# Optimization experiments

Measured on AMD Instinct MI355X. Metric: run time of the kernel, lower is better.

The kernel has to match this reference:

```python
import jax, jax.numpy as jnp
import numpy as np
import math

N_HEAD = 16
N_HEAD_KV = 4
HEAD_DIM = 128
N_EMBD = 2048

def alibi_slopes(n_heads):
    def pow2_slopes(n):
        start = 2 ** (-2 ** (-(math.log2(n) - 3)))
        return [start * start ** i for i in range(n)]
    if math.log2(n_heads).is_integer():
        return jnp.array(pow2_slopes(n_heads), dtype=jnp.float32)
    closest = 2 ** math.floor(math.log2(n_heads))
    base = pow2_slopes(closest)
    if n_heads <= 2 * closest:
        s = base + base[0::2]
    else:
        s = base + base[0::2] + base[1::2]
    return jnp.array(s[:n_heads], dtype=jnp.float32)

def setup_inputs() -> dict:
    key = jax.random.key(0)
    ks = jax.random.split(key, 5)
    B, T, C = 2, 2048, N_EMBD
    kvdim = N_HEAD_KV * HEAD_DIM
    sc = 0.02
    return {
        "x": jax.random.normal(ks[0], (B, T, C), dtype=jnp.float32),
        "q_w": jax.random.normal(ks[1], (C, C), dtype=jnp.float32) * sc,
        "k_w": jax.random.normal(ks[2], (kvdim, C), dtype=jnp.float32) * sc,
        "v_w": jax.random.normal(ks[3], (kvdim, C), dtype=jnp.float32) * sc,
        "o_w": jax.random.normal(ks[4], (C, C), dtype=jnp.float32) * sc,
    }

def reference(x, q_w, k_w, v_w, o_w):
    B, T, C = x.shape
    H, Hkv, D = N_HEAD, N_HEAD_KV, HEAD_DIM
    # nan/inf sanitize (no-op for random inputs, kept for fidelity)
    x = jnp.nan_to_num(x, nan=0.0, posinf=10000.0, neginf=-10000.0)
    q = (x @ q_w.T).reshape(B, T, H, D).transpose(0, 2, 1, 3)      # [B,H,T,D]
    k = (x @ k_w.T).reshape(B, T, Hkv, D).transpose(0, 2, 1, 3)    # [B,Hkv,T,D]
    v = (x @ v_w.T).reshape(B, T, Hkv, D).transpose(0, 2, 1, 3)
    # repeat_interleave KV heads to H heads
    rep = H // Hkv
    k = jnp.repeat(k, rep, axis=1)
    v = jnp.repeat(v, rep, axis=1)
    scale = 1.0 / math.sqrt(D)
    att = jnp.einsum('bhqd,bhkd->bhqk', q, k) * scale
    att = jnp.clip(att, -10000.0, 10000.0)
    pos = jnp.arange(T)
    causal = jnp.where(pos[None, :] > pos[:, None], -jnp.inf, 0.0)  # [T,T]
    slopes = alibi_slopes(H)  # [H]
    rel = (pos[None, :] - pos[:, None]).astype(jnp.float32)         # [T,T]
    alibi = slopes[:, None, None] * rel[None]                        # [H,T,T]
    att = att + causal[None, None] + alibi[None]
    att = jax.nn.softmax(att.astype(jnp.float32), axis=-1).astype(q.dtype)
    y = jnp.einsum('bhqk,bhkd->bhqd', att, v)
    y = jnp.nan_to_num(y, nan=0.0, posinf=10000.0, neginf=-10000.0)
    y = y.transpose(0, 2, 1, 3).reshape(B, T, C)
    return y @ o_w.T
```

## Files before the change

kernel.cpp:

```cpp
#include <hip/hip_runtime.h>
#include <hip/hip_bf16.h>
#include <math.h>

#define SEQ   2048
#define EMBD  2048
#define NH    16
#define NKV   4
#define HD    128
#define NQKV  3072
#define NUNITS 512

typedef __attribute__((ext_vector_type(8))) short short8;
typedef __attribute__((ext_vector_type(4))) short short4v;
typedef __attribute__((ext_vector_type(4))) float floatx4;

static __device__ __forceinline__ short f2bf(float f) {
    union { float f; unsigned u; } cv; cv.f = f;
    unsigned u = cv.u;
    u += 0x7FFF + ((u >> 16) & 1);
    return (short)(u >> 16);
}

#define GL16(gsrc, ldst)                                                        \
    __builtin_amdgcn_global_load_lds(                                           \
        (const __attribute__((address_space(1))) void*)(gsrc),                  \
        (__attribute__((address_space(3))) void*)(ldst), 16, 0, 0)

static __device__ __forceinline__ int alibi_window(float slope2) {
    return (int)ceilf((42.0f / slope2 + 63.0f) * (1.0f / 64.0f));
}

static __device__ __forceinline__ int unit_cost(int h, int p) {
    float slope2 = exp2f(-0.5f * (float)(h + 1)) * 1.44269504f;
    int W = alibi_window(slope2);
    return min(W + 1, 2 * p + 2);
}

__global__ void cvt_all(const float* __restrict__ x,  const float* __restrict__ qw,
                        const float* __restrict__ kw, const float* __restrict__ vw,
                        const float* __restrict__ ow,
                        short* __restrict__ xb, short* __restrict__ wall,
                        short* __restrict__ owb) {
    int i = blockIdx.x * blockDim.x + threadIdx.x;
    const float* src; short* dst; int off;
    if (i < 2097152)      { src = x;  dst = xb;             off = i; }
    else if (i < 3145728) { src = qw; dst = wall;           off = i - 2097152; }
    else if (i < 3407872) { src = kw; dst = wall + 4194304; off = i - 3145728; }
    else if (i < 3670016) { src = vw; dst = wall + 5242880; off = i - 3407872; }
    else                  { src = ow; dst = owb;            off = i - 3670016; }
    float4 v = ((const float4*)src)[off];
    float a[4] = {v.x, v.y, v.z, v.w};
    short4v o;
#pragma unroll
    for (int j = 0; j < 4; ++j) {
        float f = a[j];
        f = isnan(f) ? 0.0f : fminf(fmaxf(f, -10000.0f), 10000.0f);
        o[j] = f2bf(f);
    }
    ((short4v*)dst)[off] = o;
}

__global__ void attn_setup(int* __restrict__ qtab) {
    __shared__ int keys[NUNITS];
    int i = threadIdx.x;
    int hp = i >> 1;
    int key = unit_cost(hp >> 4, hp & 15) * 1024 + i;
    keys[i] = key;
    __syncthreads();
    int rank = 0;
    for (int j = 0; j < NUNITS; ++j) rank += (keys[j] > key);
    qtab[rank] = i;
}

template<int MODE>
__global__ __launch_bounds__(256) void gemm_bt(
    const short* __restrict__ A, const short* __restrict__ W,
    float* __restrict__ Cout, int M, int N, int K,
    short* __restrict__ qb, short* __restrict__ kb, short* __restrict__ vb)
{
    __shared__ __align__(16) short sA[128 * 64];
    __shared__ __align__(16) short sB[128 * 64];

    const int tid  = threadIdx.x;
    const int lane = tid & 63;
    const int wv   = tid >> 6;
    const int wr   = wv >> 1, wc = wv & 1;
    const int lr   = lane & 15, lg = lane >> 4;
    const int bn   = blockIdx.x, bm = blockIdx.y;

    const short* gA[4]; const short* gB[4];
    short* lA[4]; short* lB[4];
#pragma unroll
    for (int s = 0; s < 4; ++s) {
        int ck  = wv * 256 + s * 64 + lane;
        int row = ck >> 3, seg = ck & 7;
        int segSw = seg ^ (row & 7);
        gA[s] = A + (size_t)(bm * 128 + row) * K + segSw * 8;
        gB[s] = W + (size_t)(bn * 128 + row) * K + segSw * 8;
        lA[s] = &sA[(wv * 256 + s * 64) * 8];
        lB[s] = &sB[(wv * 256 + s * 64) * 8];
    }

    floatx4 acc[4][4] = {};
    const int nkt = K / 64;
    for (int kt = 0; kt < nkt; ++kt) {
#pragma unroll
        for (int s = 0; s < 4; ++s) {
            GL16(gA[s] + kt * 64, lA[s]);
            GL16(gB[s] + kt * 64, lB[s]);
        }
        __syncthreads();

#pragma unroll
        for (int ks = 0; ks < 2; ++ks) {
            short8 af[4], bfr[4];
#pragma unroll
            for (int i = 0; i < 4; ++i) {
                int ra = wr * 64 + i * 16 + lr;
                int rb = wc * 64 + i * 16 + lr;
                af[i]  = *(const short8*)&sA[ra * 64 + (((ks * 4 + lg) ^ (ra & 7)) * 8)];
                bfr[i] = *(const short8*)&sB[rb * 64 + (((ks * 4 + lg) ^ (rb & 7)) * 8)];
            }
#pragma unroll
            for (int i = 0; i < 4; ++i)
#pragma unroll
                for (int j = 0; j < 4; ++j)
                    acc[i][j] = __builtin_amdgcn_mfma_f32_16x16x32_bf16(af[i], bfr[j], acc[i][j], 0, 0, 0);
        }
        __syncthreads();
    }

    const float QSCALE = 0.08838834764831845f * 1.44269504f;
#pragma unroll
    for (int i = 0; i < 4; ++i)
#pragma unroll
        for (int j = 0; j < 4; ++j)
#pragma unroll
            for (int r = 0; r < 4; ++r) {
                int gm = bm * 128 + wr * 64 + i * 16 + lg * 4 + r;
                int gn = bn * 128 + wc * 64 + j * 16 + lr;
                float v = acc[i][j][r];
                if (MODE == 0) {
                    int b = gm >> 11, t = gm & (SEQ - 1);
                    if (gn < 2048) {
                        int h = gn >> 7, d = gn & 127;
                        qb[(((size_t)(b * NH + h)) * SEQ + t) * HD + d] = f2bf(v * QSCALE);
                    } else if (gn < 2560) {
                        int hk = (gn - 2048) >> 7, d = gn & 127;
                        kb[(((size_t)(b * NKV + hk)) * SEQ + t) * HD + d] = f2bf(v);
                    } else {
                        int hv = (gn - 2560) >> 7, d = gn & 127;
                        vb[(((size_t)(b * NKV + hv)) * HD + d) * SEQ + t] = f2bf(v);
                    }
                } else {
                    Cout[(size_t)gm * N + gn] = v;
                }
            }
}

__global__ __launch_bounds__(512, 4) void attn_fwd(
    const short* __restrict__ Q, const short* __restrict__ Kg,
    const short* __restrict__ VT, short* __restrict__ Y,
    const int* __restrict__ qtab)
{
    __shared__ __align__(16) short sK[2][64 * 128];
    __shared__ __align__(16) short sV[128 * 64];
    __shared__ short Plds[8][16][72];

    const int tid  = threadIdx.x;
    const int wave = tid >> 6, lane = tid & 63;
    const int lr = lane & 15, lg = lane >> 4;
    const int bid = blockIdx.x;

    const int rank = (bid < 256) ? bid : (767 - bid);
    const int uu = qtab[rank];
    const int b = uu & 1, hp = uu >> 1;
    const int h = hp >> 4, p = hp & 15;
    const int hkv = h >> 2;
    const int qgw = 2 * p + (wave < 4 ? 1 : 0);

    const short* Qb = Q  +  ((size_t)(b * NH  + h  )) * SEQ * HD;
    const short* Kp = Kg +  ((size_t)(b * NKV + hkv)) * SEQ * HD;
    const short* Vp = VT +  ((size_t)(b * NKV + hkv)) * HD * SEQ;

    const float slope2 = exp2f(-0.5f * (float)(h + 1)) * 1.44269504f;
    const int W = alibi_window(slope2);
    const int thi = 2 * p + 1;
    int tlo = thi - W; if (tlo < 0) tlo = 0;

    const short* gK[2]; const short* gV[2];
    int lOff[2];
#pragma unroll
    for (int j = 0; j < 2; ++j) {
        int ck = wave * 128 + j * 64 + lane;
        int krow = ck >> 4, kseg = ck & 15;
        gK[j] = Kp + (size_t)krow * HD + (kseg ^ (krow & 7)) * 8;
        int vrow = ck >> 3, vseg = ck & 7;
        gV[j] = Vp + (size_t)vrow * SEQ + (vseg ^ (vrow & 7)) * 8;
        lOff[j] = (wave * 128 + j * 64) * 8;
    }

    float c_nt[4];
#pragma unroll
    for (int nt = 0; nt < 4; ++nt) c_nt[nt] = slope2 * (float)(nt * 16 + lr);

    const int q0 = qgw * 64 + (wave & 3) * 16;
    short8 qf[4];
#pragma unroll
    for (int cc = 0; cc < 4; ++cc)
        qf[cc] = *(const short8*)&Qb[(size_t)(q0 + lr) * HD + cc * 32 + lg * 8];

    floatx4 po[8] = {};
    float m[4], lsum[4];
#pragma unroll
    for (int r = 0; r < 4; ++r) { m[r] = -3.0e38f; lsum[r] = 0.0f; }

    int cur = 0;
#pragma unroll
    for (int j = 0; j < 2; ++j)
        GL16(gK[j] + (size_t)(thi << 6) * HD, &sK[0][0] + lOff[j]);
    __syncthreads();

#pragma unroll 1
    for (int t = thi; t >= tlo; --t) {
#pragma unroll
        for (int j = 0; j < 2; ++j)
            GL16(gV[j] + (t << 6), &sV[0] + lOff[j]);
        if (t > tlo) {
#pragma unroll
            for (int j = 0; j < 2; ++j)
                GL16(gK[j] + (size_t)((t - 1) << 6) * HD, &sK[cur ^ 1][0] + lOff[j]);
        }

        const bool active = (t <= qgw) && (t > qgw - W);
        const int kv0 = t << 6;

        if (active) {
            const short* kr = &sK[cur][0];
            floatx4 sf[4];
            __builtin_amdgcn_s_setprio(1);
#pragma unroll
            for (int nt = 0; nt < 4; ++nt) {
                floatx4 sacc = {0.f, 0.f, 0.f, 0.f};
#pragma unroll
                for (int cc = 0; cc < 4; ++cc) {
                    int krow = nt * 16 + lr;
                    short8 kf = *(const short8*)&kr[krow * 128 + (((cc * 4 + lg) ^ (krow & 7)) * 8)];
                    sacc = __builtin_amdgcn_mfma_f32_16x16x32_bf16(qf[cc], kf, sacc, 0, 0, 0);
                }
                sf[nt] = sacc;
            }
            __builtin_amdgcn_s_setprio(0);

            const float a2t = slope2 * (float)kv0;
            const bool masked = (t == qgw);
#pragma unroll
            for (int r = 0; r < 4; ++r) {
                const int qpos = q0 + lg * 4 + r;
                float sv[4];
#pragma unroll
                for (int nt = 0; nt < 4; ++nt)
                    sv[nt] = sf[nt][r] + a2t + c_nt[nt];
                if (masked) {
#pragma unroll
                    for (int nt = 0; nt < 4; ++nt) {
                        int kpos = kv0 + nt * 16 + lr;
                        if (kpos > qpos) sv[nt] = -3.0e38f;
                    }
                }
                bool over = (sv[0] > m[r]) | (sv[1] > m[r]) | (sv[2] > m[r]) | (sv[3] > m[r]);
                if (__any(over)) {
                    float mx = fmaxf(fmaxf(sv[0], sv[1]), fmaxf(sv[2], sv[3]));
#pragma unroll
                    for (int off = 1; off < 16; off <<= 1) mx = fmaxf(mx, __shfl_xor(mx, off));
                    float mn = fmaxf(m[r], mx);
                    float rs = exp2f(m[r] - mn);
                    lsum[r] *= rs;
#pragma unroll
                    for (int dt = 0; dt < 8; ++dt) po[dt][r] *= rs;
                    m[r] = mn;
                }
#pragma unroll
                for (int nt = 0; nt < 4; ++nt) {
                    float pp = exp2f(sv[nt] - m[r]);
                    lsum[r] += pp;
                    Plds[wave][lg * 4 + r][nt * 16 + lr] = f2bf(pp);
                }
            }
        }

        __syncthreads();

        if (active) {
            short8 pf0 = *(const short8*)&Plds[wave][lr][lg * 8];
            short8 pf1 = *(const short8*)&Plds[wave][lr][32 + lg * 8];
            __builtin_amdgcn_s_setprio(1);
#pragma unroll
            for (int dt = 0; dt < 8; ++dt) {
                int vrow = dt * 16 + lr;
                short8 vf0 = *(const short8*)&sV[vrow * 64 + (((lg    ) ^ (vrow & 7)) * 8)];
                short8 vf1 = *(const short8*)&sV[vrow * 64 + (((lg + 4) ^ (vrow & 7)) * 8)];
                po[dt] = __builtin_amdgcn_mfma_f32_16x16x32_bf16(pf0, vf0, po[dt], 0, 0, 0);
                po[dt] = __builtin_amdgcn_mfma_f32_16x16x32_bf16(pf1, vf1, po[dt], 0, 0, 0);
            }
            __builtin_amdgcn_s_setprio(0);
        }

        __syncthreads();
        cur ^= 1;
    }

#pragma unroll
    for (int r = 0; r < 4; ++r) {
        float sum = lsum[r];
#pragma unroll
        for (int off = 1; off < 16; off <<= 1) sum += __shfl_xor(sum, off);
        float inv = 1.0f / sum;
        int row = q0 + lg * 4 + r;
#pragma unroll
        for (int dt = 0; dt < 8; ++dt)
            Y[((size_t)(b * SEQ + row)) * EMBD + h * HD + dt * 16 + lr] = f2bf(po[dt][r] * inv);
    }
}

extern "C" void kernel_launch(void* const* d_in, const int* in_sizes, int n_in,
                              void* d_out, int out_size, void* d_ws, size_t ws_size,
                              hipStream_t stream) {
    const float* x   = (const float*)d_in[0];
    const float* q_w = (const float*)d_in[1];
    const float* k_w = (const float*)d_in[2];
    const float* v_w = (const float*)d_in[3];
    const float* o_w = (const float*)d_in[4];
    float* out = (float*)d_out;

    char* ws = (char*)d_ws;
    short* x_bf  = (short*)(ws);
    short* w_all = (short*)(ws + 16777216);
    short* o_wb  = (short*)(ws + 29360128);
    short* q_b   = (short*)(ws + 37748736);
    short* k_b   = (short*)(ws + 54525952);
    short* vT_b  = (short*)(ws + 58720256);
    short* y_b   = (short*)(ws + 62914560);
    int*   qtab  = (int*)(ws);

    cvt_all<<<18432, 256, 0, stream>>>(x, q_w, k_w, v_w, o_w, x_bf, w_all, o_wb);

    gemm_bt<0><<<dim3(NQKV / 128, 4096 / 128), 256, 0, stream>>>(
        x_bf, w_all, nullptr, 4096, NQKV, EMBD, q_b, k_b, vT_b);

    attn_setup<<<1, NUNITS, 0, stream>>>(qtab);
    attn_fwd<<<512, 512, 0, stream>>>(q_b, k_b, vT_b, y_b, qtab);

    gemm_bt<1><<<dim3(EMBD / 128, 4096 / 128), 256, 0, stream>>>(
        y_b, o_wb, out, 4096, EMBD, EMBD, nullptr, nullptr, nullptr);
}
```

Measured before the change: 213.2 us.

## Split long attention units across KV and schedule them via a persistent atomic queue

The heaviest attention work units (heads with the widest ALiBi windows at late query positions) are split into two KV halves. Each half writes unnormalized partial output plus running max and sum to a workspace buffer, and a new combine kernel merges the halves. The attention kernel becomes persistent: blocks pull cost-sorted units from an atomic counter instead of using a fixed block-to-unit mapping. The goal is to shorten the load-imbalance tail, at the cost of an extra launch, partial-result traffic and atomic dispatch overhead.

```diff
diff --git a/kernel.cpp b/kernel.cpp
--- a/kernel.cpp
+++ b/kernel.cpp
@@ -8,7 +8,7 @@
 #define NKV   4
 #define HD    128
 #define NQKV  3072
-#define NUNITS 512
+#define NUNITS 584
 
 typedef __attribute__((ext_vector_type(8))) short short8;
 typedef __attribute__((ext_vector_type(4))) short short4v;
@@ -28,12 +28,6 @@
 
 static __device__ __forceinline__ int alibi_window(float slope2) {
     return (int)ceilf((42.0f / slope2 + 63.0f) * (1.0f / 64.0f));
-}
-
-static __device__ __forceinline__ int unit_cost(int h, int p) {
-    float slope2 = exp2f(-0.5f * (float)(h + 1)) * 1.44269504f;
-    int W = alibi_window(slope2);
-    return min(W + 1, 2 * p + 2);
 }
 
 __global__ void cvt_all(const float* __restrict__ x,  const float* __restrict__ qw,
@@ -62,14 +56,29 @@
 
 __global__ void attn_setup(int* __restrict__ qtab) {
     __shared__ int keys[NUNITS];
-    int i = threadIdx.x;
-    int hp = i >> 1;
-    int key = unit_cost(hp >> 4, hp & 15) * 1024 + i;
-    keys[i] = key;
+    const int i = threadIdx.x;
+    int key = 0, enc = 0;
+    if (i < NUNITS) {
+        int b, h, p, c;
+        if (i < 512) { b = i >> 8; h = (i >> 4) & 15; p = i & 15; c = 0; }
+        else { int j = i - 512; b = j / 36; int r2 = j % 36; h = 10 + r2 / 6; p = 10 + r2 % 6; c = 1; }
+        float slope2 = exp2f(-0.5f * (float)(h + 1)) * 1.44269504f;
+        int W = alibi_window(slope2);
+        int L = min(W + 1, 2 * p + 2);
+        bool split = (h >= 10) && (p >= 10);
+        int n0 = (L + 1) >> 1;
+        int cost = split ? (c == 0 ? n0 : L - n0) : L;
+        enc = (c << 9) | (b << 8) | (h << 4) | p;
+        key = cost * 1024 + i;
+        keys[i] = key;
+    }
     __syncthreads();
-    int rank = 0;
-    for (int j = 0; j < NUNITS; ++j) rank += (keys[j] > key);
-    qtab[rank] = i;
+    if (i < NUNITS) {
+        int rank = 0;
+        for (int j = 0; j < NUNITS; ++j) rank += (keys[j] > key);
+        qtab[rank] = enc;
+    }
+    if (i == 0) qtab[NUNITS] = 0;
 }
 
 template<int MODE>
@@ -161,166 +170,222 @@
 __global__ __launch_bounds__(512, 4) void attn_fwd(
     const short* __restrict__ Q, const short* __restrict__ Kg,
     const short* __restrict__ VT, short* __restrict__ Y,
-    const int* __restrict__ qtab)
+    float* __restrict__ part, int* __restrict__ qtab)
 {
     __shared__ __align__(16) short sK[2][64 * 128];
     __shared__ __align__(16) short sV[128 * 64];
     __shared__ short Plds[8][16][72];
+    __shared__ int s_unit;
 
     const int tid  = threadIdx.x;
     const int wave = tid >> 6, lane = tid & 63;
     const int lr = lane & 15, lg = lane >> 4;
-    const int bid = blockIdx.x;
-
-    const int rank = (bid < 256) ? bid : (767 - bid);
-    const int uu = qtab[rank];
-    const int b = uu & 1, hp = uu >> 1;
-    const int h = hp >> 4, p = hp & 15;
-    const int hkv = h >> 2;
-    const int qgw = 2 * p + (wave < 4 ? 1 : 0);
-
-    const short* Qb = Q  +  ((size_t)(b * NH  + h  )) * SEQ * HD;
-    const short* Kp = Kg +  ((size_t)(b * NKV + hkv)) * SEQ * HD;
-    const short* Vp = VT +  ((size_t)(b * NKV + hkv)) * HD * SEQ;
-
-    const float slope2 = exp2f(-0.5f * (float)(h + 1)) * 1.44269504f;
-    const int W = alibi_window(slope2);
-    const int thi = 2 * p + 1;
-    int tlo = thi - W; if (tlo < 0) tlo = 0;
-
-    const short* gK[2]; const short* gV[2];
+    int* qcnt = qtab + NUNITS;
+
     int lOff[2];
 #pragma unroll
-    for (int j = 0; j < 2; ++j) {
-        int ck = wave * 128 + j * 64 + lane;
-        int krow = ck >> 4, kseg = ck & 15;
-        gK[j] = Kp + (size_t)krow * HD + (kseg ^ (krow & 7)) * 8;
-        int vrow = ck >> 3, vseg = ck & 7;
-        gV[j] = Vp + (size_t)vrow * SEQ + (vseg ^ (vrow & 7)) * 8;
-        lOff[j] = (wave * 128 + j * 64) * 8;
-    }
-
-    float c_nt[4];
-#pragma unroll
-    for (int nt = 0; nt < 4; ++nt) c_nt[nt] = slope2 * (float)(nt * 16 + lr);
-
-    const int q0 = qgw * 64 + (wave & 3) * 16;
-    short8 qf[4];
-#pragma unroll
-    for (int cc = 0; cc < 4; ++cc)
-        qf[cc] = *(const short8*)&Qb[(size_t)(q0 + lr) * HD + cc * 32 + lg * 8];
-
-    floatx4 po[8] = {};
-    float m[4], lsum[4];
-#pragma unroll
-    for (int r = 0; r < 4; ++r) { m[r] = -3.0e38f; lsum[r] = 0.0f; }
-
-    int cur = 0;
-#pragma unroll
     for (int j = 0; j < 2; ++j)
-        GL16(gK[j] + (size_t)(thi << 6) * HD, &sK[0][0] + lOff[j]);
-    __syncthreads();
+        lOff[j] = (wave * 128 + j * 64 + lane) * 8;
+
+    for (;;) {
+        if (tid == 0) {
+            int r = atomicAdd(qcnt, 1);
+            s_unit = (r < NUNITS) ? qtab[r] : -1;
+        }
+        __syncthreads();
+        const int enc = s_unit;
+        __syncthreads();
+        if (enc < 0) break;
+
+        const int c = (enc >> 9) & 1, b = (enc >> 8) & 1;
+        const int h = (enc >> 4) & 15, p = enc & 15;
+        const int hkv = h >> 2;
+        const int qgw = 2 * p + (wave < 4 ? 1 : 0);
+
+        const short* Qb = Q  +  ((size_t)(b * NH  + h  )) * SEQ * HD;
+        const short* Kp = Kg +  ((size_t)(b * NKV + hkv)) * SEQ * HD;
+        const short* Vp = VT +  ((size_t)(b * NKV + hkv)) * HD * SEQ;
+
+        const float slope2 = exp2f(-0.5f * (float)(h + 1)) * 1.44269504f;
+        const int W = alibi_window(slope2);
+        const int thi = 2 * p + 1;
+        const int L = min(W + 1, 2 * p + 2);
+        const bool split = (h >= 10) && (p >= 10);
+        const int n0 = (L + 1) >> 1;
+        int t1, t0;
+        if (!split)      { t1 = thi;      t0 = thi - L + 1; }
+        else if (c == 0) { t1 = thi;      t0 = thi - n0 + 1; }
+        else             { t1 = thi - n0; t0 = thi - L + 1; }
+
+        const short* gK[2]; const short* gV[2];
+#pragma unroll
+        for (int j = 0; j < 2; ++j) {
+            int ck = wave * 128 + j * 64 + lane;
+            int krow = ck >> 4, kseg = ck & 15;
+            gK[j] = Kp + (size_t)krow * HD + (kseg ^ (krow & 7)) * 8;
+            int vrow = ck >> 3, vseg = ck & 7;
+            gV[j] = Vp + (size_t)vrow * SEQ + (vseg ^ (vrow & 7)) * 8;
+        }
+
+        float c_nt[4];
+#pragma unroll
+        for (int nt = 0; nt < 4; ++nt) c_nt[nt] = slope2 * (float)(nt * 16 + lr);
+
+        const int q0 = qgw * 64 + (wave & 3) * 16;
+        short8 qf[4];
+#pragma unroll
+        for (int cc = 0; cc < 4; ++cc)
+            qf[cc] = *(const short8*)&Qb[(size_t)(q0 + lr) * HD + cc * 32 + lg * 8];
+
+        floatx4 po[8] = {};
+        float m[4], lsum[4];
+#pragma unroll
+        for (int r = 0; r < 4; ++r) { m[r] = -3.0e38f; lsum[r] = 0.0f; }
+
+        int cur = 0;
+#pragma unroll
+        for (int j = 0; j < 2; ++j)
+            GL16(gK[j] + (size_t)(t1 << 6) * HD, &sK[0][0] + lOff[j]);
+        __syncthreads();
 
 #pragma unroll 1
-    for (int t = thi; t >= tlo; --t) {
-#pragma unroll
-        for (int j = 0; j < 2; ++j)
-            GL16(gV[j] + (t << 6), &sV[0] + lOff[j]);
-        if (t > tlo) {
+        for (int t = t1; t >= t0; --t) {
 #pragma unroll
             for (int j = 0; j < 2; ++j)
-                GL16(gK[j] + (size_t)((t - 1) << 6) * HD, &sK[cur ^ 1][0] + lOff[j]);
-        }
-
-        const bool active = (t <= qgw) && (t > qgw - W);
-        const int kv0 = t << 6;
-
-        if (active) {
-            const short* kr = &sK[cur][0];
-            floatx4 sf[4];
-            __builtin_amdgcn_s_setprio(1);
-#pragma unroll
-            for (int nt = 0; nt < 4; ++nt) {
-                floatx4 sacc = {0.f, 0.f, 0.f, 0.f};
-#pragma unroll
-                for (int cc = 0; cc < 4; ++cc) {
-                    int krow = nt * 16 + lr;
-                    short8 kf = *(const short8*)&kr[krow * 128 + (((cc * 4 + lg) ^ (krow & 7)) * 8)];
-                    sacc = __builtin_amdgcn_mfma_f32_16x16x32_bf16(qf[cc], kf, sacc, 0, 0, 0);
+                GL16(gV[j] + (t << 6), &sV[0] + lOff[j]);
+            if (t > t0) {
+#pragma unroll
+                for (int j = 0; j < 2; ++j)
+                    GL16(gK[j] + (size_t)((t - 1) << 6) * HD, &sK[cur ^ 1][0] + lOff[j]);
+            }
+
+            const bool active = (t <= qgw) && (t > qgw - W);
+            const int kv0 = t << 6;
+
+            if (active) {
+                const short* kr = &sK[cur][0];
+                floatx4 sf[4];
+                __builtin_amdgcn_s_setprio(1);
+#pragma unroll
+                for (int nt = 0; nt < 4; ++nt) {
+                    floatx4 sacc = {0.f, 0.f, 0.f, 0.f};
+#pragma unroll
+                    for (int cc = 0; cc < 4; ++cc) {
+                        int krow = nt * 16 + lr;
+                        short8 kf = *(const short8*)&kr[krow * 128 + (((cc * 4 + lg) ^ (krow & 7)) * 8)];
+                        sacc = __builtin_amdgcn_mfma_f32_16x16x32_bf16(qf[cc], kf, sacc, 0, 0, 0);
+                    }
+                    sf[nt] = sacc;
                 }
-                sf[nt] = sacc;
-            }
-            __builtin_amdgcn_s_setprio(0);
-
-            const float a2t = slope2 * (float)kv0;
-            const bool masked = (t == qgw);
-#pragma unroll
-            for (int r = 0; r < 4; ++r) {
-                const int qpos = q0 + lg * 4 + r;
-                float sv[4];
-#pragma unroll
-                for (int nt = 0; nt < 4; ++nt)
-                    sv[nt] = sf[nt][r] + a2t + c_nt[nt];
-                if (masked) {
+                __builtin_amdgcn_s_setprio(0);
+
+                const float a2t = slope2 * (float)kv0;
+                const bool masked = (t == qgw);
+#pragma unroll
+                for (int r = 0; r < 4; ++r) {
+                    const int qpos = q0 + lg * 4 + r;
+                    float sv[4];
+#pragma unroll
+                    for (int nt = 0; nt < 4; ++nt)
+                        sv[nt] = sf[nt][r] + a2t + c_nt[nt];
+                    if (masked) {
+#pragma unroll
+                        for (int nt = 0; nt < 4; ++nt) {
+                            int kpos = kv0 + nt * 16 + lr;
+                            if (kpos > qpos) sv[nt] = -3.0e38f;
+                        }
+                    }
+                    bool over = (sv[0] > m[r]) | (sv[1] > m[r]) | (sv[2] > m[r]) | (sv[3] > m[r]);
+                    if (__any(over)) {
+                        float mx = fmaxf(fmaxf(sv[0], sv[1]), fmaxf(sv[2], sv[3]));
+#pragma unroll
+                        for (int off = 1; off < 16; off <<= 1) mx = fmaxf(mx, __shfl_xor(mx, off));
+                        float mn = fmaxf(m[r], mx);
+                        float rs = exp2f(m[r] - mn);
+                        lsum[r] *= rs;
+#pragma unroll
+                        for (int dt = 0; dt < 8; ++dt) po[dt][r] *= rs;
+                        m[r] = mn;
+                    }
 #pragma unroll
                     for (int nt = 0; nt < 4; ++nt) {
-                        int kpos = kv0 + nt * 16 + lr;
-                        if (kpos > qpos) sv[nt] = -3.0e38f;
+                        float pp = exp2f(sv[nt] - m[r]);
+                        lsum[r] += pp;
+                        Plds[wave][lg * 4 + r][nt * 16 + lr] = f2bf(pp);
                     }
                 }
-                bool over = (sv[0] > m[r]) | (sv[1] > m[r]) | (sv[2] > m[r]) | (sv[3] > m[r]);
-                if (__any(over)) {
-                    float mx = fmaxf(fmaxf(sv[0], sv[1]), fmaxf(sv[2], sv[3]));
-#pragma unroll
-                    for (int off = 1; off < 16; off <<= 1) mx = fmaxf(mx, __shfl_xor(mx, off));
-                    float mn = fmaxf(m[r], mx);
-                    float rs = exp2f(m[r] - mn);
-                    lsum[r] *= rs;
-#pragma unroll
-                    for (int dt = 0; dt < 8; ++dt) po[dt][r] *= rs;
-                    m[r] = mn;
+            }
+
+            __syncthreads();
+
+            if (active) {
+                short8 pf0 = *(const short8*)&Plds[wave][lr][lg * 8];
+                short8 pf1 = *(const short8*)&Plds[wave][lr][32 + lg * 8];
+                __builtin_amdgcn_s_setprio(1);
+#pragma unroll
+                for (int dt = 0; dt < 8; ++dt) {
+                    int vrow = dt * 16 + lr;
+                    short8 vf0 = *(const short8*)&sV[vrow * 64 + (((lg    ) ^ (vrow & 7)) * 8)];
+                    short8 vf1 = *(const short8*)&sV[vrow * 64 + (((lg + 4) ^ (vrow & 7)) * 8)];
+                    po[dt] = __builtin_amdgcn_mfma_f32_16x16x32_bf16(pf0, vf0, po[dt], 0, 0, 0);
+                    po[dt] = __builtin_amdgcn_mfma_f32_16x16x32_bf16(pf1, vf1, po[dt], 0, 0, 0);
                 }
-#pragma unroll
-                for (int nt = 0; nt < 4; ++nt) {
-                    float pp = exp2f(sv[nt] - m[r]);
-                    lsum[r] += pp;
-                    Plds[wave][lg * 4 + r][nt * 16 + lr] = f2bf(pp);
-                }
-            }
-        }
-
-        __syncthreads();
-
-        if (active) {
-            short8 pf0 = *(const short8*)&Plds[wave][lr][lg * 8];
-            short8 pf1 = *(const short8*)&Plds[wave][lr][32 + lg * 8];
-            __builtin_amdgcn_s_setprio(1);
-#pragma unroll
-            for (int dt = 0; dt < 8; ++dt) {
-                int vrow = dt * 16 + lr;
-                short8 vf0 = *(const short8*)&sV[vrow * 64 + (((lg    ) ^ (vrow & 7)) * 8)];
-                short8 vf1 = *(const short8*)&sV[vrow * 64 + (((lg + 4) ^ (vrow & 7)) * 8)];
-                po[dt] = __builtin_amdgcn_mfma_f32_16x16x32_bf16(pf0, vf0, po[dt], 0, 0, 0);
-                po[dt] = __builtin_amdgcn_mfma_f32_16x16x32_bf16(pf1, vf1, po[dt], 0, 0, 0);
-            }
-            __builtin_amdgcn_s_setprio(0);
-        }
-
-        __syncthreads();
-        cur ^= 1;
-    }
-
-#pragma unroll
-    for (int r = 0; r < 4; ++r) {
-        float sum = lsum[r];
-#pragma unroll
-        for (int off = 1; off < 16; off <<= 1) sum += __shfl_xor(sum, off);
-        float inv = 1.0f / sum;
-        int row = q0 + lg * 4 + r;
-#pragma unroll
-        for (int dt = 0; dt < 8; ++dt)
-            Y[((size_t)(b * SEQ + row)) * EMBD + h * HD + dt * 16 + lr] = f2bf(po[dt][r] * inv);
-    }
+                __builtin_amdgcn_s_setprio(0);
+            }
+
+            __syncthreads();
+            cur ^= 1;
+        }
+
+        if (!split) {
+#pragma unroll
+            for (int r = 0; r < 4; ++r) {
+                float sum = lsum[r];
+#pragma unroll
+                for (int off = 1; off < 16; off <<= 1) sum += __shfl_xor(sum, off);
+                float inv = 1.0f / sum;
+                int row = q0 + lg * 4 + r;
+#pragma unroll
+                for (int dt = 0; dt < 8; ++dt)
+                    Y[((size_t)(b * SEQ + row)) * EMBD + h * HD + dt * 16 + lr] = f2bf(po[dt][r] * inv);
+            }
+        } else {
+            int jslot = b * 36 + (h - 10) * 6 + (p - 10);
+            float* pw = part + (size_t)(jslot * 2 + c) * (128 * 130);
+#pragma unroll
+            for (int r = 0; r < 4; ++r) {
+                float sum = lsum[r];
+#pragma unroll
+                for (int off = 1; off < 16; off <<= 1) sum += __shfl_xor(sum, off);
+                int rr = wave * 16 + lg * 4 + r;
+#pragma unroll
+                for (int dt = 0; dt < 8; ++dt)
+                    pw[rr * 130 + dt * 16 + lr] = po[dt][r];
+                if (lr == 0) { pw[rr * 130 + 128] = m[r]; pw[rr * 130 + 129] = sum; }
+            }
+        }
+    }
+}
+
+__global__ void attn_combine(const float* __restrict__ part, short* __restrict__ Y) {
+    const int tid = threadIdx.x;
+    const int rg  = blockIdx.x * 2 + (tid >> 7);
+    const int col = tid & 127;
+    const int j = rg >> 7, rr = rg & 127;
+    const int b = j / 36; const int r2 = j % 36;
+    const int h = 10 + r2 / 6, p = 10 + r2 % 6;
+
+    const float* p0 = part + ((size_t)(j * 2) * 128 + rr) * 130;
+    const float* p1 = p0 + 128 * 130;
+    float m0 = p0[128], l0 = p0[129];
+    float m1 = p1[128], l1 = p1[129];
+    float M = fmaxf(m0, m1);
+    float s0 = exp2f(m0 - M), s1 = exp2f(m1 - M);
+    float v = (p0[col] * s0 + p1[col] * s1) / (l0 * s0 + l1 * s1);
+
+    const int w = rr >> 4, i2 = rr & 15;
+    const int grow = (w < 4 ? (2 * p + 1) : (2 * p)) * 64 + (w & 3) * 16 + i2;
+    Y[((size_t)(b * SEQ + grow)) * EMBD + h * HD + col] = f2bf(v);
 }
 
 extern "C" void kernel_launch(void* const* d_in, const int* in_sizes, int n_in,
@@ -342,14 +407,16 @@
     short* vT_b  = (short*)(ws + 58720256);
     short* y_b   = (short*)(ws + 62914560);
     int*   qtab  = (int*)(ws);
+    float* part  = (float*)(ws + 65536);
 
     cvt_all<<<18432, 256, 0, stream>>>(x, q_w, k_w, v_w, o_w, x_bf, w_all, o_wb);
 
     gemm_bt<0><<<dim3(NQKV / 128, 4096 / 128), 256, 0, stream>>>(
         x_bf, w_all, nullptr, 4096, NQKV, EMBD, q_b, k_b, vT_b);
 
-    attn_setup<<<1, NUNITS, 0, stream>>>(qtab);
-    attn_fwd<<<512, 512, 0, stream>>>(q_b, k_b, vT_b, y_b, qtab);
+    attn_setup<<<1, 640, 0, stream>>>(qtab);
+    attn_fwd<<<512, 512, 0, stream>>>(q_b, k_b, vT_b, y_b, part, qtab);
+    attn_combine<<<4608, 256, 0, stream>>>(part, y_b);
 
     gemm_bt<1><<<dim3(EMBD / 128, 4096 / 128), 256, 0, stream>>>(
         y_b, o_wb, out, 4096, EMBD, EMBD, nullptr, nullptr, nullptr);
```

New measurement: 208.7 us. 2.2% less time.
